# Kernel optimization log

Measured on AMD Instinct MI355X. Metric: run time of the kernel, lower is better.

Reference implementation:

```python
import jax, jax.numpy as jnp
import numpy as np

B, L, DIM, H, D, WS = 2, 2048, 1024, 16, 64, 256
SCALE = D ** -0.5


def _rope_tables(seq_len, dim, dtype):
    inv_freq = 1.0 / (10000.0 ** (jnp.arange(0, dim, 2, dtype=jnp.float32) / dim))
    t = jnp.arange(seq_len, dtype=jnp.float32)
    freqs = jnp.einsum('i,j->ij', t, inv_freq)          # [L, D/2]
    emb = jnp.concatenate([freqs, freqs], axis=-1)       # [L, D]
    return jnp.cos(emb).astype(dtype), jnp.sin(emb).astype(dtype)


def _rotate_half(x):
    x1, x2 = x[..., : x.shape[-1] // 2], x[..., x.shape[-1] // 2:]
    return jnp.concatenate([-x2, x1], axis=-1)


def _apply_rope(t, cos, sin):
    # t: [B, L, H, D]; cos/sin: [L, D] broadcast over batch and heads
    return t * cos[None, :, None, :] + _rotate_half(t) * sin[None, :, None, :]


def setup_inputs() -> dict:
    key = jax.random.key(0)
    k0, k1, k2 = jax.random.split(key, 3)
    x = jax.random.normal(k0, (B, L, DIM), dtype=jnp.float32)
    Wqkv = jax.random.normal(k1, (3 * H * D, DIM), dtype=jnp.float32) * 0.02
    bqkv = jnp.zeros((3 * H * D,), dtype=jnp.float32)
    Wproj = jax.random.normal(k2, (DIM, H * D), dtype=jnp.float32) * 0.02
    bproj = jnp.zeros((DIM,), dtype=jnp.float32)
    return {"x": x, "Wqkv": Wqkv, "bqkv": bqkv, "Wproj": Wproj, "bproj": bproj, "is_global": 1}


def _attention(x, Wqkv, bqkv, Wproj, bproj, is_global):
    b, l, _ = x.shape
    qkv = x @ Wqkv.T + bqkv                              # [B, L, 3*H*D]
    q, k, v = jnp.split(qkv, 3, axis=-1)
    q, k, v = (t.reshape(b, l, H, D) for t in (q, k, v))
    cos, sin = _rope_tables(l, D, x.dtype)
    q = _apply_rope(q, cos, sin)
    k = _apply_rope(k, cos, sin)
    if is_global:
        attn = jnp.einsum('bshd,bthd->bhst', q, k) * SCALE
        attn = jax.nn.softmax(attn, axis=-1)
        out = jnp.einsum('bhst,bthd->bshd', attn, v)     # [B, L, H, D]
    else:
        pad = (WS - l % WS) % WS
        if pad > 0:
            q, k, v = (jnp.pad(t, ((0, 0), (0, pad), (0, 0), (0, 0))) for t in (q, k, v))
        w = (l + pad) // WS
        q = q.reshape(b, w, WS, H, D)
        k = k.reshape(b, w, WS, H, D)
        v = v.reshape(b, w, WS, H, D)
        attn = jnp.einsum('bwshd,bwthd->bwhst', q, k) * SCALE
        attn = jax.nn.softmax(attn, axis=-1)
        out = jnp.einsum('bwhst,bwthd->bwshd', attn, v).reshape(b, w * WS, H, D)
        out = out[:, :l]
    return out.reshape(b, l, H * D) @ Wproj.T + bproj


def reference(x, Wqkv, bqkv, Wproj, bproj, is_global):
    return _attention(x, Wqkv, bqkv, Wproj, bproj, is_global)
```

## Files before the change

kernel.cpp:

```cpp
#include <hip/hip_runtime.h>
#include <math.h>

#define NB 2
#define NL 2048
#define NDIM 1024
#define NH 16
#define ND 64
#define NWS 256
#define NM (NB*NL)
#define QSCALE 0.18033688011112042f

typedef __attribute__((ext_vector_type(8))) short short8;
typedef __attribute__((ext_vector_type(4))) float f32x4;
typedef unsigned short ushort_t;
typedef unsigned int uint_t;

#define MFMA16(a,b,acc) __builtin_amdgcn_mfma_f32_16x16x32_bf16((a),(b),(acc),0,0,0)

static __device__ __forceinline__ ushort_t f2bf(float x){
    uint_t u = __float_as_uint(x);
    uint_t r = (u + 0x7fff + ((u >> 16) & 1)) >> 16;
    return (ushort_t)r;
}
static __device__ __forceinline__ float bf2f(ushort_t u){
    return __uint_as_float(((uint_t)u) << 16);
}
static __device__ __forceinline__ float fast_exp2(float x){
#if __has_builtin(__builtin_amdgcn_exp2f)
    return __builtin_amdgcn_exp2f(x);
#else
    return exp2f(x);
#endif
}

static __device__ __forceinline__ void async_load16(const void* g, void* l){
    __builtin_amdgcn_global_load_lds(
        (const __attribute__((address_space(1))) unsigned int*)g,
        (__attribute__((address_space(3))) unsigned int*)l, 16, 0, 0);
}

__launch_bounds__(256)
__global__ void split_all(const float* __restrict__ x,  ushort_t* __restrict__ xh,  ushort_t* __restrict__ xl,
                          const float* __restrict__ wq, ushort_t* __restrict__ wqh, ushort_t* __restrict__ wql,
                          const float* __restrict__ wp, ushort_t* __restrict__ wph, ushort_t* __restrict__ wpl)
{
    int i = blockIdx.x*256 + threadIdx.x;
    const float* in; ushort_t *oh, *ol;
    if (i < 1048576)      { in = x;  oh = xh;  ol = xl;  }
    else if (i < 1835008) { in = wq; oh = wqh; ol = wql; i -= 1048576; }
    else                  { in = wp; oh = wph; ol = wpl; i -= 1835008; }
    const int e = i*4;
    const float4 v = *(const float4*)(in + e);
    ushort_t h0=f2bf(v.x), h1=f2bf(v.y), h2=f2bf(v.z), h3=f2bf(v.w);
    ushort4 h4; h4.x=h0; h4.y=h1; h4.z=h2; h4.w=h3;
    ushort4 l4;
    l4.x=f2bf(v.x - bf2f(h0)); l4.y=f2bf(v.y - bf2f(h1));
    l4.z=f2bf(v.z - bf2f(h2)); l4.w=f2bf(v.w - bf2f(h3));
    *(ushort4*)(oh + e) = h4;
    *(ushort4*)(ol + e) = l4;
}

__launch_bounds__(256)
__global__ void rope_tab(float* __restrict__ tc, float* __restrict__ ts)
{
    const int idx = blockIdx.x*256 + threadIdx.x;
    const int j = idx >> 11, l = idx & (NL-1);
    const float invf = 1.0f / powf(10000.0f, (float)j * (1.0f/32.0f));
    float s, c;
    sincosf((float)l * invf, &s, &c);
    tc[idx] = c; ts[idx] = s;
}

__launch_bounds__(256, 3)
__global__ void gemm_qkv(const ushort_t* __restrict__ Ah, const ushort_t* __restrict__ Al,
                         const ushort_t* __restrict__ Bh,
                         const float* __restrict__ bias,
                         ushort_t* __restrict__ oQh, ushort_t* __restrict__ oKh,
                         ushort_t* __restrict__ oVth,
                         const float* __restrict__ tcos, const float* __restrict__ tsin)
{
    __shared__ __align__(16) char smem[50176];
    ushort_t* sA_h = (ushort_t*)smem;
    ushort_t* sA_l = (ushort_t*)(smem + 8192);
    ushort_t* sB_h = (ushort_t*)(smem + 16384);
    ushort_t* sBounce = (ushort_t*)smem;
    const int ebuf = 12288;
    const int bbuf = 24576;

    const int tid  = threadIdx.x;
    const int wv   = tid >> 6, lane = tid & 63;
    const int quad = lane >> 4, l16 = lane & 15;
    const int m0 = blockIdx.y << 7, n0 = blockIdx.x << 7;
    const int wr = wv >> 1, wc = wv & 1;

    const ushort_t* gsrc;
    ushort_t* lds_base;
    int rowb, npass;
    if (wv == 0)      { gsrc = Ah; lds_base = sA_h; rowb = m0; npass = 8; }
    else if (wv == 1) { gsrc = Al; lds_base = sA_l; rowb = m0; npass = 8; }
    else { gsrc = Bh; lds_base = sB_h + (wv-2)*64*32; rowb = n0 + (wv-2)*64; npass = 4; }
    const int rl = lane >> 2;
    const int cp = lane & 3;
    const int cg = cp ^ ((rl >> 1) & 3);
    const ushort_t* gptr = gsrc + (size_t)(rowb + rl)*NDIM + cg*8;

    f32x4 acc[4][4];
    #pragma unroll
    for (int i=0;i<4;++i)
        #pragma unroll
        for (int j=0;j<4;++j) acc[i][j] = (f32x4){0.f,0.f,0.f,0.f};

    const int swz = (l16 >> 1) & 3;
    const int ac_off = (wr*64 + l16)*32 + ((quad ^ swz) << 3);
    const int bc_off = (wc*64 + l16)*32 + ((quad ^ swz) << 3);

#define QSTAGE(BUF, KOFF) do { \
        const ushort_t* gp_ = gptr + (KOFF); \
        for (int p=0; p<npass; ++p) \
            async_load16(gp_ + (size_t)p*16*NDIM, (char*)lds_base + (BUF)*bbuf + p*1024); \
    } while(0)

#define QCOMP(BUF) do { \
        const int eo_ = (BUF)*ebuf; \
        short8 ah[4], al[4], bh[4]; \
        _Pragma("unroll") \
        for (int t=0;t<4;++t){ \
            ah[t] = *(const short8*)&sA_h[eo_ + t*512 + ac_off]; \
            al[t] = *(const short8*)&sA_l[eo_ + t*512 + ac_off]; \
            bh[t] = *(const short8*)&sB_h[eo_ + t*512 + bc_off]; \
        } \
        _Pragma("unroll") \
        for (int mt=0;mt<4;++mt) \
            _Pragma("unroll") \
            for (int nt=0;nt<4;++nt){ \
                f32x4 a_ = acc[mt][nt]; \
                a_ = MFMA16(ah[mt], bh[nt], a_); \
                a_ = MFMA16(al[mt], bh[nt], a_); \
                acc[mt][nt] = a_; \
            } \
    } while(0)

    QSTAGE(0, 0);
    for (int k0 = 0; k0 < NDIM; k0 += 64) {
        __syncthreads();
        QSTAGE(1, k0 + 32);
        QCOMP(0);
        __syncthreads();
        if (k0 + 64 < NDIM) QSTAGE(0, k0 + 64);
        QCOMP(1);
    }
#undef QSTAGE
#undef QCOMP

    const int colb = n0 + wc*64;
    const int sel  = colb >> 10;
    const int head = (colb & 1023) >> 6;
    float bq[4];
    #pragma unroll
    for (int nt=0;nt<4;++nt) bq[nt] = bias[colb + nt*16 + l16];

    if (sel == 2) {
        __syncthreads();
        const int bb = m0 >> 11;
        const int Lb = (m0 & (NL-1)) + wr*64;
        ushort_t* sT = sBounce + wv*(64*72);
        const size_t gb = ((size_t)(bb*NH + head)*ND)*NL + Lb;
        const int drow = lane >> 3, dcol = lane & 7;
        #pragma unroll
        for (int mt=0;mt<4;++mt)
            #pragma unroll
            for (int nt=0;nt<4;++nt)
                #pragma unroll
                for (int r=0;r<4;++r)
                    sT[(nt*16+l16)*72 + mt*16 + quad*4 + r] = f2bf(acc[mt][nt][r] + bq[nt]);
        #pragma unroll
        for (int dd=0; dd<8; ++dd){
            const int d = dd*8 + drow;
            const uint4 v = *(const uint4*)&sT[d*72 + dcol*8];
            *(uint4*)(oVth + gb + (size_t)d*NL + dcol*8) = v;
        }
    } else {
        ushort_t* dh = sel ? oKh : oQh;
        const float qs = sel ? 1.0f : QSCALE;
        #pragma unroll
        for (int mt=0;mt<4;++mt)
            #pragma unroll
            for (int r=0;r<4;++r){
                const int m = m0 + wr*64 + mt*16 + quad*4 + r;
                const int bb = m >> 11, l = m & (NL-1);
                const size_t ro = ((size_t)((bb*NH + head)*NL + l)) << 6;
                #pragma unroll
                for (int ntp=0;ntp<2;++ntp){
                    const int j = ntp*16 + l16;
                    const float c = tcos[j*NL + l];
                    const float s = tsin[j*NL + l];
                    const float x1 = acc[mt][ntp  ][r] + bq[ntp];
                    const float x2 = acc[mt][ntp+2][r] + bq[ntp+2];
                    const int d1 = ntp*16 + l16;
                    dh[ro + d1]      = f2bf((x1*c - x2*s) * qs);
                    dh[ro + d1 + 32] = f2bf((x2*c + x1*s) * qs);
                }
            }
    }
}

__launch_bounds__(256, 2)
__global__ void gemm_proj(const ushort_t* __restrict__ Ah, const ushort_t* __restrict__ Al,
                          const ushort_t* __restrict__ Bh, const ushort_t* __restrict__ Bl,
                          const float* __restrict__ bias,
                          float* __restrict__ Cout)
{
    __shared__ __align__(16) char smem[74752];
    ushort_t* sA_h = (ushort_t*)smem;
    ushort_t* sA_l = (ushort_t*)(smem + 8192);
    ushort_t* sB_h = (ushort_t*)(smem + 16384);
    ushort_t* sB_l = (ushort_t*)(smem + 20480);
    const int ebuf = 12288;
    const int bbuf = 24576;

    const int tid  = threadIdx.x;
    const int wv   = tid >> 6, lane = tid & 63;
    const int quad = lane >> 4, l16 = lane & 15;
    const int m0 = blockIdx.y << 7, n0 = blockIdx.x << 6;
    const int wr = wv >> 1, wc = wv & 1;

    const int rl = lane >> 2;
    const int cp = lane & 3;
    const int cg = cp ^ ((rl >> 1) & 3);
    const ushort_t* pAh = Ah + (size_t)(m0 + 32*wv + rl)*NDIM + cg*8;
    const ushort_t* pAl = Al + (size_t)(m0 + 32*wv + rl)*NDIM + cg*8;
    const ushort_t* pBh = Bh + (size_t)(n0 + 16*wv + rl)*NDIM + cg*8;
    const ushort_t* pBl = Bl + (size_t)(n0 + 16*wv + rl)*NDIM + cg*8;
    char* dA  = smem + wv*2048;
    char* dB0 = smem + 16384 + wv*1024;
    char* dB1 = smem + 20480 + wv*1024;

    f32x4 acc[4][2];
    #pragma unroll
    for (int i=0;i<4;++i)
        #pragma unroll
        for (int j=0;j<2;++j) acc[i][j] = (f32x4){0.f,0.f,0.f,0.f};

    const int swz = (l16 >> 1) & 3;
    const int ac_off = (wr*64 + l16)*32 + ((quad ^ swz) << 3);
    const int bc_off = (wc*32 + l16)*32 + ((quad ^ swz) << 3);

#define PSTAGE(SLOT, KOFF) do { \
        const int so_ = (SLOT)*bbuf; \
        async_load16(pAh + (KOFF),           dA + so_); \
        async_load16(pAh + 16*NDIM + (KOFF), dA + so_ + 1024); \
        async_load16(pAl + (KOFF),           dA + so_ + 8192); \
        async_load16(pAl + 16*NDIM + (KOFF), dA + so_ + 9216); \
        async_load16(pBh + (KOFF), dB0 + so_); \
        async_load16(pBl + (KOFF), dB1 + so_); \
    } while(0)

#define PCOMP(SLOT) do { \
        const int eo_ = (SLOT)*ebuf; \
        short8 ah[4], al[4], bh[2], bl[2]; \
        _Pragma("unroll") \
        for (int t=0;t<4;++t){ \
            ah[t] = *(const short8*)&sA_h[eo_ + t*512 + ac_off]; \
            al[t] = *(const short8*)&sA_l[eo_ + t*512 + ac_off]; \
        } \
        _Pragma("unroll") \
        for (int t=0;t<2;++t){ \
            bh[t] = *(const short8*)&sB_h[eo_ + t*512 + bc_off]; \
            bl[t] = *(const short8*)&sB_l[eo_ + t*512 + bc_off]; \
        } \
        _Pragma("unroll") \
        for (int mt=0;mt<4;++mt) \
            _Pragma("unroll") \
            for (int nt=0;nt<2;++nt){ \
                f32x4 a_ = acc[mt][nt]; \
                a_ = MFMA16(ah[mt], bh[nt], a_); \
                a_ = MFMA16(al[mt], bh[nt], a_); \
                a_ = MFMA16(ah[mt], bl[nt], a_); \
                acc[mt][nt] = a_; \
            } \
    } while(0)

#define PPHASE(SLOT, K0, VN) do { \
        asm volatile("s_waitcnt vmcnt(" #VN ")" ::: "memory"); \
        __builtin_amdgcn_sched_barrier(0); \
        __builtin_amdgcn_s_barrier(); \
        __builtin_amdgcn_sched_barrier(0); \
        PCOMP(SLOT); \
        asm volatile("s_waitcnt lgkmcnt(0)" ::: "memory"); \
        __builtin_amdgcn_sched_barrier(0); \
        __builtin_amdgcn_s_barrier(); \
        __builtin_amdgcn_sched_barrier(0); \
        if ((K0) + 96 < NDIM) PSTAGE(SLOT, (K0) + 96); \
    } while(0)

    PSTAGE(0, 0); PSTAGE(1, 32); PSTAGE(2, 64);
    for (int k0 = 0; k0 < 960; k0 += 96) {
        PPHASE(0, k0,      12);
        PPHASE(1, k0 + 32, 12);
        PPHASE(2, k0 + 64, 12);
    }
    PPHASE(0, 960, 0);
    PPHASE(1, 992, 0);
#undef PSTAGE
#undef PCOMP
#undef PPHASE

    const int colb = n0 + wc*32;
    float bq[2];
    #pragma unroll
    for (int nt=0;nt<2;++nt) bq[nt] = bias[colb + nt*16 + l16];
    #pragma unroll
    for (int mt=0;mt<4;++mt)
        #pragma unroll
        for (int r=0;r<4;++r){
            const int m = m0 + wr*64 + mt*16 + quad*4 + r;
            float* orow = Cout + (size_t)m*NDIM + colb;
            #pragma unroll
            for (int nt=0;nt<2;++nt)
                orow[nt*16 + l16] = acc[mt][nt][r] + bq[nt];
        }
}

__launch_bounds__(256, 3)
__global__ void attn_mfma(const ushort_t* __restrict__ Qh,
                          const ushort_t* __restrict__ Kh,
                          const ushort_t* __restrict__ Vth,
                          ushort_t* __restrict__ AOh, ushort_t* __restrict__ AOl,
                          const int* __restrict__ isg)
{
    __shared__ __align__(16) char smem[49152];

    const int tid  = threadIdx.x;
    const int wv   = tid >> 6, lane = tid & 63;
    const int quad = lane >> 4, l16 = lane & 15;
    const int bh = blockIdx.x & 31, qt = blockIdx.x >> 5;
    const int q0w = qt*128 + wv*32;

    short8 bq[2][2];
    {
        const size_t rb = (((size_t)bh*NL + q0w) << 6);
        #pragma unroll
        for (int mt=0; mt<2; ++mt)
            #pragma unroll
            for (int c=0; c<2; ++c)
                bq[mt][c] = *(const short8*)(Qh + rb + (size_t)((mt*16 + l16) << 6) + quad*8 + c*32);
    }
    short8 ones;
    #pragma unroll
    for (int j=0;j<8;++j) ones[j] = (short)0x3F80;

    f32x4 o[2][4];
    #pragma unroll
    for (int mt=0; mt<2; ++mt)
        #pragma unroll
        for (int dnt=0; dnt<4; ++dnt)
            o[mt][dnt] = (f32x4){0.f,0.f,0.f,0.f};
    f32x4 lsacc[2] = {(f32x4){0.f,0.f,0.f,0.f}, (f32x4){0.f,0.f,0.f,0.f}};

    const int gflag = isg[0];
    int klo, khi;
    if (gflag) { klo = 0; khi = NL; }
    else       { klo = (qt >> 1)*NWS; khi = klo + NWS; }

    const int swz4 = (l16 & 7) << 4;
    const int KC0 = l16*128 + (( quad*16      ) ^ swz4);
    const int KC1 = l16*128 + (( quad*16 + 64 ) ^ swz4);
    const int sPb = 32768 + wv*4096;
    int PW[4];
    #pragma unroll
    for (int knt=0; knt<4; ++knt)
        PW[knt] = sPb + l16*128 + ((knt*32 + quad*8) ^ swz4);
    const int PR0 = sPb + KC0;
    const int PR1 = sPb + KC1;

    const int r8  = lane >> 3;
    const int c8s = (lane & 7) ^ r8;
    const ushort_t* Kp = Kh + (((size_t)bh*NL) << 6)
                       + (size_t)(klo + wv*16 + r8)*64 + c8s*8;
    const ushort_t* Vp = Vth + (size_t)bh*ND*NL
                       + (size_t)(wv*16 + r8)*NL + klo + c8s*8;
    const int kdst = wv*2048;
    const int vdst = 16384 + wv*2048;

#define STAGE(BUF) do { \
        async_load16(Kp,          smem + (BUF)*8192 + kdst); \
        async_load16(Kp + 512,    smem + (BUF)*8192 + kdst + 1024); \
        async_load16(Vp,          smem + (BUF)*8192 + vdst); \
        async_load16(Vp + 8*NL,   smem + (BUF)*8192 + vdst + 1024); \
        Kp += 64*64; Vp += 64; } while (0)

#define TILE(BUF) do { \
        const char* kb_ = smem + (BUF)*8192; \
        const char* vb_ = smem + 16384 + (BUF)*8192; \
        f32x4 s0_[4], s1_[4]; \
        _Pragma("unroll") \
        for (int knt=0; knt<4; ++knt) { \
            const short8 a0 = *(const short8*)(kb_ + knt*2048 + KC0); \
            const short8 a1 = *(const short8*)(kb_ + knt*2048 + KC1); \
            f32x4 t0 = (f32x4){0.f,0.f,0.f,0.f}; \
            t0 = MFMA16(a0, bq[0][0], t0); \
            t0 = MFMA16(a1, bq[0][1], t0); \
            s0_[knt] = t0; \
            f32x4 t1 = (f32x4){0.f,0.f,0.f,0.f}; \
            t1 = MFMA16(a0, bq[1][0], t1); \
            t1 = MFMA16(a1, bq[1][1], t1); \
            s1_[knt] = t1; \
        } \
        short8 fp[2][2]; \
        _Pragma("unroll") \
        for (int mt=0; mt<2; ++mt) { \
            _Pragma("unroll") \
            for (int knt=0; knt<4; ++knt) { \
                const f32x4 sv = mt ? s1_[knt] : s0_[knt]; \
                const uint_t u0 = __float_as_uint(fast_exp2(sv[0])); \
                const uint_t u1 = __float_as_uint(fast_exp2(sv[1])); \
                const uint_t u2 = __float_as_uint(fast_exp2(sv[2])); \
                const uint_t u3 = __float_as_uint(fast_exp2(sv[3])); \
                uint2 pk_; \
                pk_.x = __builtin_amdgcn_perm(u1, u0, 0x07060302u); \
                pk_.y = __builtin_amdgcn_perm(u3, u2, 0x07060302u); \
                *(uint2*)(smem + mt*2048 + PW[knt]) = pk_; \
            } \
            fp[mt][0] = *(const short8*)(smem + mt*2048 + PR0); \
            fp[mt][1] = *(const short8*)(smem + mt*2048 + PR1); \
            lsacc[mt] = MFMA16(fp[mt][0], ones, lsacc[mt]); \
            lsacc[mt] = MFMA16(fp[mt][1], ones, lsacc[mt]); \
        } \
        _Pragma("unroll") \
        for (int dnt=0; dnt<4; ++dnt) { \
            const short8 v0 = *(const short8*)(vb_ + dnt*2048 + KC0); \
            const short8 v1 = *(const short8*)(vb_ + dnt*2048 + KC1); \
            _Pragma("unroll") \
            for (int mt=0; mt<2; ++mt) { \
                f32x4 t = o[mt][dnt]; \
                t = MFMA16(fp[mt][0], v0, t); \
                t = MFMA16(fp[mt][1], v1, t); \
                o[mt][dnt] = t; \
            } \
        } } while (0)

    STAGE(0);
    for (int kt = klo; kt < khi; kt += 128) {
        __syncthreads();
        if (kt + 64 < khi) STAGE(1);
        TILE(0);
        __syncthreads();
        if (kt + 128 < khi) STAGE(0);
        TILE(1);
    }
#undef STAGE
#undef TILE

    const int bb = bh >> 4, hh = bh & 15;
    #pragma unroll
    for (int mt=0; mt<2; ++mt)
        #pragma unroll
        for (int r=0; r<4; ++r) {
            const float inv = 1.0f / lsacc[mt][r];
            const int row = q0w + mt*16 + quad*4 + r;
            const size_t ob = (((size_t)(bb*NL + row)) << 10) + (hh << 6);
            #pragma unroll
            for (int dnt=0; dnt<4; ++dnt) {
                const float val = o[mt][dnt][r] * inv;
                const ushort_t h = f2bf(val);
                AOh[ob + dnt*16 + l16] = h;
                AOl[ob + dnt*16 + l16] = f2bf(val - bf2f(h));
            }
        }
}

extern "C" void kernel_launch(void* const* d_in, const int* in_sizes, int n_in,
                              void* d_out, int out_size, void* d_ws, size_t ws_size,
                              hipStream_t stream)
{
    const float* x     = (const float*)d_in[0];
    const float* Wqkv  = (const float*)d_in[1];
    const float* bqkv  = (const float*)d_in[2];
    const float* Wproj = (const float*)d_in[3];
    const float* bproj = (const float*)d_in[4];
    const int*   isg   = (const int*)d_in[5];
    float* out = (float*)d_out;
    char* base = (char*)d_ws;

    const size_t MB = 1024*1024;
    ushort_t* Qh  = (ushort_t*)(base);
    ushort_t* Kh  = (ushort_t*)(base + 16*MB);
    ushort_t* Vth = (ushort_t*)(base + 32*MB);
    ushort_t* xh  = (ushort_t*)(base + 48*MB);
    ushort_t* xl  = (ushort_t*)(base + 56*MB);
    ushort_t* AOh = xh;
    ushort_t* AOl = xl;
    ushort_t* Wqh = (ushort_t*)(base + 64*MB);
    ushort_t* Wql = (ushort_t*)(base + 64*MB + 6291456);
    ushort_t* Wph = (ushort_t*)(base + 76*MB);
    ushort_t* Wpl = (ushort_t*)(base + 76*MB + 2097152);
    float*    tcs = (float*)(base + 80*MB);
    float*    tsn = (float*)(base + 80*MB + 262144);

    split_all<<<8192, 256, 0, stream>>>(x, xh, xl, Wqkv, Wqh, Wql, Wproj, Wph, Wpl);
    rope_tab<<<256, 256, 0, stream>>>(tcs, tsn);

    gemm_qkv<<<dim3(3*NDIM/128, NM/128), 256, 0, stream>>>(
        xh, xl, Wqh, bqkv, Qh, Kh, Vth, tcs, tsn);

    attn_mfma<<<NB*NH*(NL/128), 256, 0, stream>>>(
        Qh, Kh, Vth, AOh, AOl, isg);

    gemm_proj<<<dim3(NDIM/64, NM/128), 256, 0, stream>>>(
        AOh, AOl, Wph, Wpl, bproj, out);
}
```

Baseline: 212.7 us.

## Triple-buffer attention K/V loads with vmcnt waits and fuse rope table into split

The attention kernel's double-buffered K/V staging becomes a three-slot ring. Explicit s_waitcnt vmcnt counts let two tiles' loads stay in flight while the current tile is computed, with raw s_barrier calls in place of __syncthreads. The goal is to hide global-load latency behind MFMA work, at the cost of 64KB LDS and lowering occupancy to 2 blocks per CU. Separately, the rope table kernel is merged into the split kernel as extra blocks to save one launch.

```diff
diff --git a/kernel.cpp b/kernel.cpp
--- a/kernel.cpp
+++ b/kernel.cpp
@@ -40,35 +40,35 @@
 }
 
 __launch_bounds__(256)
-__global__ void split_all(const float* __restrict__ x,  ushort_t* __restrict__ xh,  ushort_t* __restrict__ xl,
-                          const float* __restrict__ wq, ushort_t* __restrict__ wqh, ushort_t* __restrict__ wql,
-                          const float* __restrict__ wp, ushort_t* __restrict__ wph, ushort_t* __restrict__ wpl)
+__global__ void split_rope(const float* __restrict__ x,  ushort_t* __restrict__ xh,  ushort_t* __restrict__ xl,
+                           const float* __restrict__ wq, ushort_t* __restrict__ wqh, ushort_t* __restrict__ wql,
+                           const float* __restrict__ wp, ushort_t* __restrict__ wph, ushort_t* __restrict__ wpl,
+                           float* __restrict__ tc, float* __restrict__ ts)
 {
-    int i = blockIdx.x*256 + threadIdx.x;
-    const float* in; ushort_t *oh, *ol;
-    if (i < 1048576)      { in = x;  oh = xh;  ol = xl;  }
-    else if (i < 1835008) { in = wq; oh = wqh; ol = wql; i -= 1048576; }
-    else                  { in = wp; oh = wph; ol = wpl; i -= 1835008; }
-    const int e = i*4;
-    const float4 v = *(const float4*)(in + e);
-    ushort_t h0=f2bf(v.x), h1=f2bf(v.y), h2=f2bf(v.z), h3=f2bf(v.w);
-    ushort4 h4; h4.x=h0; h4.y=h1; h4.z=h2; h4.w=h3;
-    ushort4 l4;
-    l4.x=f2bf(v.x - bf2f(h0)); l4.y=f2bf(v.y - bf2f(h1));
-    l4.z=f2bf(v.z - bf2f(h2)); l4.w=f2bf(v.w - bf2f(h3));
-    *(ushort4*)(oh + e) = h4;
-    *(ushort4*)(ol + e) = l4;
-}
-
-__launch_bounds__(256)
-__global__ void rope_tab(float* __restrict__ tc, float* __restrict__ ts)
-{
-    const int idx = blockIdx.x*256 + threadIdx.x;
-    const int j = idx >> 11, l = idx & (NL-1);
-    const float invf = 1.0f / powf(10000.0f, (float)j * (1.0f/32.0f));
-    float s, c;
-    sincosf((float)l * invf, &s, &c);
-    tc[idx] = c; ts[idx] = s;
+    const int b = blockIdx.x;
+    if (b < 8192) {
+        int i = b*256 + threadIdx.x;
+        const float* in; ushort_t *oh, *ol;
+        if (i < 1048576)      { in = x;  oh = xh;  ol = xl;  }
+        else if (i < 1835008) { in = wq; oh = wqh; ol = wql; i -= 1048576; }
+        else                  { in = wp; oh = wph; ol = wpl; i -= 1835008; }
+        const int e = i*4;
+        const float4 v = *(const float4*)(in + e);
+        ushort_t h0=f2bf(v.x), h1=f2bf(v.y), h2=f2bf(v.z), h3=f2bf(v.w);
+        ushort4 h4; h4.x=h0; h4.y=h1; h4.z=h2; h4.w=h3;
+        ushort4 l4;
+        l4.x=f2bf(v.x - bf2f(h0)); l4.y=f2bf(v.y - bf2f(h1));
+        l4.z=f2bf(v.z - bf2f(h2)); l4.w=f2bf(v.w - bf2f(h3));
+        *(ushort4*)(oh + e) = h4;
+        *(ushort4*)(ol + e) = l4;
+    } else {
+        const int idx = (b - 8192)*256 + threadIdx.x;
+        const int j = idx >> 11, l = idx & (NL-1);
+        const float invf = 1.0f / powf(10000.0f, (float)j * (1.0f/32.0f));
+        float s, c;
+        sincosf((float)l * invf, &s, &c);
+        tc[idx] = c; ts[idx] = s;
+    }
 }
 
 __launch_bounds__(256, 3)
@@ -321,14 +321,14 @@
         }
 }
 
-__launch_bounds__(256, 3)
+__launch_bounds__(256, 2)
 __global__ void attn_mfma(const ushort_t* __restrict__ Qh,
                           const ushort_t* __restrict__ Kh,
                           const ushort_t* __restrict__ Vth,
                           ushort_t* __restrict__ AOh, ushort_t* __restrict__ AOl,
                           const int* __restrict__ isg)
 {
-    __shared__ __align__(16) char smem[49152];
+    __shared__ __align__(16) char smem[65536];
 
     const int tid  = threadIdx.x;
     const int wv   = tid >> 6, lane = tid & 63;
@@ -365,7 +365,7 @@
     const int swz4 = (l16 & 7) << 4;
     const int KC0 = l16*128 + (( quad*16      ) ^ swz4);
     const int KC1 = l16*128 + (( quad*16 + 64 ) ^ swz4);
-    const int sPb = 32768 + wv*4096;
+    const int sPb = 49152 + wv*4096;
     int PW[4];
     #pragma unroll
     for (int knt=0; knt<4; ++knt)
@@ -380,18 +380,19 @@
     const ushort_t* Vp = Vth + (size_t)bh*ND*NL
                        + (size_t)(wv*16 + r8)*NL + klo + c8s*8;
     const int kdst = wv*2048;
-    const int vdst = 16384 + wv*2048;
-
-#define STAGE(BUF) do { \
-        async_load16(Kp,          smem + (BUF)*8192 + kdst); \
-        async_load16(Kp + 512,    smem + (BUF)*8192 + kdst + 1024); \
-        async_load16(Vp,          smem + (BUF)*8192 + vdst); \
-        async_load16(Vp + 8*NL,   smem + (BUF)*8192 + vdst + 1024); \
+    const int vdst = 8192 + wv*2048;
+
+#define ASTAGE(SLOT) do { \
+        char* sb_ = smem + (SLOT)*16384; \
+        async_load16(Kp,          sb_ + kdst); \
+        async_load16(Kp + 512,    sb_ + kdst + 1024); \
+        async_load16(Vp,          sb_ + vdst); \
+        async_load16(Vp + 8*NL,   sb_ + vdst + 1024); \
         Kp += 64*64; Vp += 64; } while (0)
 
-#define TILE(BUF) do { \
-        const char* kb_ = smem + (BUF)*8192; \
-        const char* vb_ = smem + 16384 + (BUF)*8192; \
+#define ATILE(SLOT) do { \
+        const char* kb_ = smem + (SLOT)*16384; \
+        const char* vb_ = kb_ + 8192; \
         f32x4 s0_[4], s1_[4]; \
         _Pragma("unroll") \
         for (int knt=0; knt<4; ++knt) { \
@@ -439,17 +440,33 @@
             } \
         } } while (0)
 
-    STAGE(0);
-    for (int kt = klo; kt < khi; kt += 128) {
-        __syncthreads();
-        if (kt + 64 < khi) STAGE(1);
-        TILE(0);
-        __syncthreads();
-        if (kt + 128 < khi) STAGE(0);
-        TILE(1);
+#define APHASE(SLOT, VN) do { \
+        asm volatile("s_waitcnt vmcnt(" #VN ")" ::: "memory"); \
+        __builtin_amdgcn_sched_barrier(0); \
+        __builtin_amdgcn_s_barrier(); \
+        __builtin_amdgcn_sched_barrier(0); \
+        ATILE(SLOT); \
+        asm volatile("s_waitcnt lgkmcnt(0)" ::: "memory"); \
+        __builtin_amdgcn_sched_barrier(0); \
+        __builtin_amdgcn_s_barrier(); \
+        __builtin_amdgcn_sched_barrier(0); \
+        if (next_kt < khi) ASTAGE(SLOT); \
+        next_kt += 64; } while (0)
+
+    const int nt = (khi - klo) >> 6;
+    ASTAGE(0); ASTAGE(1); ASTAGE(2);
+    int next_kt = klo + 192;
+    int slot = 0;
+    for (int i = 0; i < nt - 2; ++i) {
+        APHASE(slot, 8);
+        slot = (slot == 2) ? 0 : slot + 1;
     }
-#undef STAGE
-#undef TILE
+    APHASE(slot, 4);
+    slot = (slot == 2) ? 0 : slot + 1;
+    APHASE(slot, 0);
+#undef ASTAGE
+#undef ATILE
+#undef APHASE
 
     const int bb = bh >> 4, hh = bh & 15;
     #pragma unroll
@@ -497,8 +514,7 @@
     float*    tcs = (float*)(base + 80*MB);
     float*    tsn = (float*)(base + 80*MB + 262144);
 
-    split_all<<<8192, 256, 0, stream>>>(x, xh, xl, Wqkv, Wqh, Wql, Wproj, Wph, Wpl);
-    rope_tab<<<256, 256, 0, stream>>>(tcs, tsn);
+    split_rope<<<8448, 256, 0, stream>>>(x, xh, xl, Wqkv, Wqh, Wql, Wproj, Wph, Wpl, tcs, tsn);
 
     gemm_qkv<<<dim3(3*NDIM/128, NM/128), 256, 0, stream>>>(
         xh, xl, Wqh, bqkv, Qh, Kh, Vth, tcs, tsn);
```

After: 215.8 us. No clear change (+1.5%).
